# Kernel tuning notes

Measured on AMD Instinct MI355X. Metric: run time of the kernel, lower is better.

## Reference

```python
import jax, jax.numpy as jnp
import numpy as np

S, B, D, H = 2048, 2, 1024, 16
DK = D // H  # 64

def setup_inputs() -> dict:
    key0 = jax.random.key(0)
    ks = jax.random.split(key0, 11)
    scale = 0.02
    inp = {
        'query': jax.random.normal(ks[0], (S, B, D), jnp.float32),
        'key':   jax.random.normal(ks[1], (S, B, D), jnp.float32),
        'value': jax.random.normal(ks[2], (S, B, D), jnp.float32),
        # nn.Linear weights stored torch-style [out_features, in_features]
        'Wq': jax.random.normal(ks[3], (H * DK, D), jnp.float32) * scale,
        'bq': jnp.zeros((H * DK,), jnp.float32),
        'Wk': jax.random.normal(ks[4], (H * DK, D), jnp.float32) * scale,
        'bk': jnp.zeros((H * DK,), jnp.float32),
        'Wv': jax.random.normal(ks[5], (H * DK, D), jnp.float32) * scale,
        'bv': jnp.zeros((H * DK,), jnp.float32),
        'Wo': jax.random.normal(ks[6], (D, D), jnp.float32) * scale,
        'bo': jnp.zeros((D,), jnp.float32),
    }
    return inp

def _proj(x, W, b):
    # x: [S,B,D] -> [S,B,H,DK]
    y = jnp.einsum('sbd,ed->sbe', x, W) + b
    return y.reshape(x.shape[0], x.shape[1], H, DK)

def reference(query, key, value, Wq, bq, Wk, bk, Wv, bv, Wo, bo):
    q = _proj(query, Wq, bq)   # [S,B,H,DK]
    k = _proj(key,   Wk, bk)
    v = _proj(value, Wv, bv)
    # NOTE: original forward never applies self.scale -> unscaled QK^T (faithful)
    scores = jnp.einsum('ibhd,jbhd->ijbh', q, k)      # [Sq,Sk,B,H]
    attn = jax.nn.softmax(scores, axis=1)             # softmax over key axis j
    x = jnp.einsum('ijbh,jbhd->ibhd', attn, v)        # [S,B,H,DK]
    x = x.reshape(q.shape[0], q.shape[1], H * DK)     # [S,B,D]
    out = jnp.einsum('sbd,ed->sbe', x, Wo) + bo       # [S,B,D]
    return out
```

## Files before the change

### kernel.cpp

```cpp
#include <hip/hip_runtime.h>
#include <stdint.h>

#define S_LEN  2048
#define BATCH  2
#define DMODEL 1024
#define NHEAD  16
#define DKH    64

typedef __attribute__((ext_vector_type(8))) __bf16 bf16x8;
typedef __attribute__((ext_vector_type(4))) float  f32x4;
typedef unsigned short u16;
typedef unsigned int   u32;

#if __has_builtin(__builtin_amdgcn_exp2f)
#define EXP2(x) __builtin_amdgcn_exp2f(x)
#else
#define EXP2(x) __expf(0.69314718055994531f * (x))
#endif

#define SWAP32(a, b) asm("v_permlane32_swap_b32 %0, %1" : "+v"(a), "+v"(b))
#define SWAP16(a, b) asm("v_permlane16_swap_b32 %0, %1" : "+v"(a), "+v"(b))

__device__ __forceinline__ u16 f2bf(float f) {
  union { float f; u32 u; } v; v.f = f;
  u32 r = v.u + 0x7fffu + ((v.u >> 16) & 1u);
  return (u16)(r >> 16);
}

__global__ void cvt_all(const float4* __restrict__ q, const float4* __restrict__ k,
                        const float4* __restrict__ v,
                        const float4* __restrict__ wq, const float4* __restrict__ wk,
                        const float4* __restrict__ wv, const float4* __restrict__ wo,
                        ushort4* __restrict__ dst) {
  const int NX4 = (S_LEN * BATCH * DMODEL) / 4;
  const int NW4 = (DMODEL * DMODEL) / 4;
  int i = blockIdx.x * blockDim.x + threadIdx.x;
  const float4* src;
  int off;
  if (i < 3 * NX4) {
    src = (i < NX4) ? q : (i < 2 * NX4) ? k : v;
    off = i & (NX4 - 1);
  } else {
    int j = i - 3 * NX4;
    int t = j >> 18;
    src = (t == 0) ? wq : (t == 1) ? wk : (t == 2) ? wv : wo;
    off = j & (NW4 - 1);
  }
  float4 val = src[off];
  ushort4 o;
  o.x = f2bf(val.x); o.y = f2bf(val.y); o.z = f2bf(val.z); o.w = f2bf(val.w);
  dst[i] = o;
}

__global__ __launch_bounds__(256, 2)
void gemm_qkv(const u16* __restrict__ Abase, const u16* __restrict__ Wbase,
              const float* __restrict__ b0, const float* __restrict__ b1,
              const float* __restrict__ b2, u16* __restrict__ Obase) {
  __shared__ __align__(16) u16 As[128 * 32];
  __shared__ __align__(16) u16 Bs[128 * 32];

  const int L = blockIdx.x + (blockIdx.y << 3) + (blockIdx.z << 8);
  const int xcd = L & 7, sl = L >> 3;
  const int z  = sl >> 5;
  const int y  = xcd * 4 + ((sl >> 3) & 3);
  const int nx = sl & 7;

  const u16* A = Abase + (size_t)z * (S_LEN * BATCH * DMODEL);
  const u16* W = Wbase + (size_t)z * (DMODEL * DMODEL);
  const float* bias = (z == 0) ? b0 : (z == 1) ? b1 : b2;
  u16* O = Obase + (size_t)z * (S_LEN * BATCH * DMODEL);
  const float scl = (z == 0) ? 1.4426950408889634f : 1.0f;

  const int tid  = threadIdx.x;
  const int wave = tid >> 6, lane = tid & 63;
  const int quad = lane >> 4, lcol = lane & 15;
  const int m0 = y * 128, n0 = nx * 128;
  const int wm = (wave >> 1) * 64, wn = (wave & 1) * 64;

  f32x4 acc[4][4] = {};

  for (int k0 = 0; k0 < DMODEL; k0 += 32) {
#pragma unroll
    for (int r = 0; r < 2; ++r) {
      int idx = r * 256 + tid;
      int row = idx >> 2, col = (idx & 3) * 8;
      const u16* gA = A + (size_t)(m0 + row) * DMODEL + k0 + col;
      const u16* gW = W + (size_t)(n0 + row) * DMODEL + k0 + col;
      u16* lA = As + (size_t)(r * 256 + (tid & 192)) * 8;
      u16* lB = Bs + (size_t)(r * 256 + (tid & 192)) * 8;
      __builtin_amdgcn_global_load_lds((const __attribute__((address_space(1))) void*)gA,
                                       (__attribute__((address_space(3))) void*)lA, 16, 0, 0);
      __builtin_amdgcn_global_load_lds((const __attribute__((address_space(1))) void*)gW,
                                       (__attribute__((address_space(3))) void*)lB, 16, 0, 0);
    }
    __syncthreads();

    const u16* aBase = As + (wm + lcol) * 32 + quad * 8;
    const u16* bBase = Bs + (wn + lcol) * 32 + quad * 8;
    bf16x8 af[4], bfr[4];
#pragma unroll
    for (int i = 0; i < 4; ++i) af[i]  = *(const bf16x8*)(aBase + i * 16 * 32);
#pragma unroll
    for (int j = 0; j < 4; ++j) bfr[j] = *(const bf16x8*)(bBase + j * 16 * 32);
#pragma unroll
    for (int i = 0; i < 4; ++i)
#pragma unroll
      for (int j = 0; j < 4; ++j)
        acc[i][j] = __builtin_amdgcn_mfma_f32_16x16x32_bf16(af[i], bfr[j], acc[i][j], 0, 0, 0);
    __syncthreads();
  }

#pragma unroll
  for (int i = 0; i < 4; ++i) {
#pragma unroll
    for (int j = 0; j < 4; ++j) {
      int n = n0 + wn + j * 16 + lcol;
      int h = n >> 6, dk = n & 63;
      float bv = bias[n];
#pragma unroll
      for (int r = 0; r < 4; ++r) {
        int m = m0 + wm + i * 16 + quad * 4 + r;
        int s = m >> 1, b = m & 1;
        O[((size_t)(b * NHEAD + h) * S_LEN + s) * DKH + dk] = f2bf((acc[i][j][r] + bv) * scl);
      }
    }
  }
}

__global__ __launch_bounds__(256, 2)
void gemm_o(const u16* __restrict__ A, const u16* __restrict__ W,
            const float* __restrict__ bias, float* __restrict__ O) {
  __shared__ __align__(16) u16 As[128 * 32];
  __shared__ __align__(16) u16 Bs[64 * 32];

  const int L = blockIdx.x + (blockIdx.y << 4);
  const int xcd = L & 7, sl = L >> 3;
  const int y = xcd * 4 + (sl >> 4);
  const int x = sl & 15;

  const int tid  = threadIdx.x;
  const int wave = tid >> 6, lane = tid & 63;
  const int quad = lane >> 4, lcol = lane & 15;
  const int m0 = y * 128, n0 = x * 64;
  const int wm = (wave >> 1) * 64, wn = (wave & 1) * 32;

  f32x4 acc[4][2] = {};

  for (int k0 = 0; k0 < DMODEL; k0 += 32) {
#pragma unroll
    for (int r = 0; r < 2; ++r) {
      int idx = r * 256 + tid;
      int row = idx >> 2, col = (idx & 3) * 8;
      const u16* gA = A + (size_t)(m0 + row) * DMODEL + k0 + col;
      u16* lA = As + (size_t)(r * 256 + (tid & 192)) * 8;
      __builtin_amdgcn_global_load_lds((const __attribute__((address_space(1))) void*)gA,
                                       (__attribute__((address_space(3))) void*)lA, 16, 0, 0);
    }
    {
      int row = tid >> 2, col = (tid & 3) * 8;
      const u16* gW = W + (size_t)(n0 + row) * DMODEL + k0 + col;
      u16* lB = Bs + (size_t)(tid & 192) * 8;
      __builtin_amdgcn_global_load_lds((const __attribute__((address_space(1))) void*)gW,
                                       (__attribute__((address_space(3))) void*)lB, 16, 0, 0);
    }
    __syncthreads();

    const u16* aBase = As + (wm + lcol) * 32 + quad * 8;
    const u16* bBase = Bs + (wn + lcol) * 32 + quad * 8;
    bf16x8 af[4], bfr[2];
#pragma unroll
    for (int i = 0; i < 4; ++i) af[i]  = *(const bf16x8*)(aBase + i * 16 * 32);
#pragma unroll
    for (int j = 0; j < 2; ++j) bfr[j] = *(const bf16x8*)(bBase + j * 16 * 32);
#pragma unroll
    for (int i = 0; i < 4; ++i)
#pragma unroll
      for (int j = 0; j < 2; ++j)
        acc[i][j] = __builtin_amdgcn_mfma_f32_16x16x32_bf16(af[i], bfr[j], acc[i][j], 0, 0, 0);
    __syncthreads();
  }

#pragma unroll
  for (int i = 0; i < 4; ++i) {
#pragma unroll
    for (int j = 0; j < 2; ++j) {
      int n = n0 + wn + j * 16 + lcol;
      float bv = bias[n];
#pragma unroll
      for (int r = 0; r < 4; ++r) {
        int m = m0 + wm + i * 16 + quad * 4 + r;
        O[(size_t)m * DMODEL + n] = acc[i][j][r] + bv;
      }
    }
  }
}

__global__ __launch_bounds__(512, 4)
void attn_kernel(const u16* __restrict__ Q, const u16* __restrict__ K,
                 const u16* __restrict__ V, u16* __restrict__ O) {
  __shared__ __align__(16) u16 Ks[2][128 * 64];
  __shared__ __align__(16) u16 Vts[2][2 * 4608];
  __shared__ float ls2[4][2][16];

  const int tid  = threadIdx.x;
  const int wave = tid >> 6, lane = tid & 63;
  const int quad = lane >> 4, lcol = lane & 15;
  const int qg = wave & 3;
  const int kh = wave >> 2;

  const int L = blockIdx.x + (blockIdx.y << 4);
  const int xcd = L & 7, slot = L >> 3;
  const int bh = xcd * 4 + (slot >> 4);
  const int q0 = (slot & 15) * 128;

  const size_t headOff = (size_t)bh * S_LEN * DKH;
  const u16* Qg = Q + headOff;
  const u16* Kg = K + headOff;
  const u16* Vg = V + headOff;

  bf16x8 qf[2][2];
#pragma unroll
  for (int s = 0; s < 2; ++s)
#pragma unroll
    for (int kc = 0; kc < 2; ++kc)
      qf[s][kc] = *(const bf16x8*)(Qg + (size_t)(q0 + qg * 32 + s * 16 + lcol) * DKH +
                                   kc * 32 + quad * 8);

  const int krow = tid >> 3;
  const int kcs  = (((tid & 7) ^ ((tid >> 3) & 7))) * 8;
  const int kdst = (tid & 448) * 8;
  const int vhalf = lane >> 5, vkp = lane & 31, vo = wave;

  {
    const u16* vp = Vg + (size_t)(vhalf * (S_LEN / 2) + 2 * vkp) * DKH + 8 * vo;
    uint4 vr0 = *(const uint4*)vp;
    uint4 vr1 = *(const uint4*)(vp + DKH);
    __builtin_amdgcn_global_load_lds(
        (const __attribute__((address_space(1))) void*)(Kg + (size_t)krow * DKH + kcs),
        (__attribute__((address_space(3))) void*)(Ks[0] + kdst), 16, 0, 0);
    __builtin_amdgcn_global_load_lds(
        (const __attribute__((address_space(1))) void*)(Kg + (size_t)(S_LEN / 2 + krow) * DKH + kcs),
        (__attribute__((address_space(3))) void*)(Ks[0] + 4096 + kdst), 16, 0, 0);
    u16* vd = Vts[0] + vhalf * 4608;
#pragma unroll
    for (int jj = 0; jj < 4; ++jj) {
      u32 aw = ((const u32*)&vr0)[jj], bw = ((const u32*)&vr1)[jj];
      *(u32*)(vd + (size_t)(8 * vo + 2 * jj) * 72 + 2 * vkp)     = __builtin_amdgcn_perm(bw, aw, 0x05040100u);
      *(u32*)(vd + (size_t)(8 * vo + 2 * jj + 1) * 72 + 2 * vkp) = __builtin_amdgcn_perm(bw, aw, 0x07060302u);
    }
  }

  f32x4 o_acc[2][4] = {};
  float lsum[2] = {0.f, 0.f};

  for (int it = 0; it < 16; ++it) {
    const int cur = it & 1;
    __syncthreads();

    uint4 vr0, vr1;
    const bool has = (it < 15);
    if (has) {
      const int nb = (it + 1) * 64;
      const u16* vp = Vg + (size_t)(vhalf * (S_LEN / 2) + nb + 2 * vkp) * DKH + 8 * vo;
      vr0 = *(const uint4*)vp;
      vr1 = *(const uint4*)(vp + DKH);
      __builtin_amdgcn_global_load_lds(
          (const __attribute__((address_space(1))) void*)(Kg + (size_t)(nb + krow) * DKH + kcs),
          (__attribute__((address_space(3))) void*)(Ks[cur ^ 1] + kdst), 16, 0, 0);
      __builtin_amdgcn_global_load_lds(
          (const __attribute__((address_space(1))) void*)(Kg + (size_t)(S_LEN / 2 + nb + krow) * DKH + kcs),
          (__attribute__((address_space(3))) void*)(Ks[cur ^ 1] + 4096 + kdst), 16, 0, 0);
    }

    const u16* kb = Ks[cur] + kh * 4096;
    const u16* vb = Vts[cur] + kh * 4608;

#pragma unroll
    for (int g = 0; g < 2; ++g) {
      bf16x8 ak[2][2];
#pragma unroll
      for (int jb = 0; jb < 2; ++jb)
#pragma unroll
        for (int kc = 0; kc < 2; ++kc)
          ak[jb][kc] = *(const bf16x8*)(kb + (g * 32 + jb * 16 + lcol) * 64 +
                                        ((((kc << 2) | quad) ^ (lcol & 7)) << 3));
      f32x4 sc[2][2] = {};
      __builtin_amdgcn_s_setprio(1);
#pragma unroll
      for (int kc = 0; kc < 2; ++kc)
#pragma unroll
        for (int jb = 0; jb < 2; ++jb)
#pragma unroll
          for (int s = 0; s < 2; ++s)
            sc[jb][s] = __builtin_amdgcn_mfma_f32_16x16x32_bf16(ak[jb][kc], qf[s][kc], sc[jb][s], 0, 0, 0);
      __builtin_amdgcn_s_setprio(0);

      bf16x8 pa[2];
#pragma unroll
      for (int s = 0; s < 2; ++s) {
        u32 ww[2][2];
#pragma unroll
        for (int jb = 0; jb < 2; ++jb) {
          float p0 = EXP2(sc[jb][s][0]);
          float p1 = EXP2(sc[jb][s][1]);
          float p2 = EXP2(sc[jb][s][2]);
          float p3 = EXP2(sc[jb][s][3]);
          lsum[s] += (p0 + p1) + (p2 + p3);
          asm("v_cvt_pk_bf16_f32 %0, %1, %2" : "=v"(ww[jb][0]) : "v"(p0), "v"(p1));
          asm("v_cvt_pk_bf16_f32 %0, %1, %2" : "=v"(ww[jb][1]) : "v"(p2), "v"(p3));
        }
        u32 a0 = ww[0][0], b0 = ww[1][0];
        SWAP32(a0, b0); SWAP16(a0, b0);
        u32 a1 = ww[0][1], b1 = ww[1][1];
        SWAP32(a1, b1); SWAP16(a1, b1);
        union { u32 u[4]; bf16x8 v; } f;
        f.u[0] = a0; f.u[1] = a1; f.u[2] = b0; f.u[3] = b1;
        pa[s] = f.v;
      }

      bf16x8 bv[4];
#pragma unroll
      for (int jd = 0; jd < 4; ++jd)
        bv[jd] = *(const bf16x8*)(vb + (jd * 16 + lcol) * 72 + g * 32 + quad * 8);
      __builtin_amdgcn_s_setprio(1);
#pragma unroll
      for (int s = 0; s < 2; ++s)
#pragma unroll
        for (int jd = 0; jd < 4; ++jd)
          o_acc[s][jd] = __builtin_amdgcn_mfma_f32_16x16x32_bf16(pa[s], bv[jd], o_acc[s][jd], 0, 0, 0);
      __builtin_amdgcn_s_setprio(0);
    }

    if (has) {
      u16* vd = Vts[cur ^ 1] + vhalf * 4608;
#pragma unroll
      for (int jj = 0; jj < 4; ++jj) {
        u32 aw = ((const u32*)&vr0)[jj], bw = ((const u32*)&vr1)[jj];
        *(u32*)(vd + (size_t)(8 * vo + 2 * jj) * 72 + 2 * vkp)     = __builtin_amdgcn_perm(bw, aw, 0x05040100u);
        *(u32*)(vd + (size_t)(8 * vo + 2 * jj + 1) * 72 + 2 * vkp) = __builtin_amdgcn_perm(bw, aw, 0x07060302u);
      }
    }
  }

  __syncthreads();

#pragma unroll
  for (int s = 0; s < 2; ++s) {
    lsum[s] += __shfl_xor(lsum[s], 16);
    lsum[s] += __shfl_xor(lsum[s], 32);
  }

  float* scr = (float*)Vts;
  const int cbase = (qg * 64 + lane) * 36;
  if (kh == 1) {
#pragma unroll
    for (int s = 0; s < 2; ++s)
#pragma unroll
      for (int jd = 0; jd < 4; ++jd)
        *(f32x4*)(scr + cbase + (s * 4 + jd) * 4) = o_acc[s][jd];
    if (lane < 16) {
#pragma unroll
      for (int s = 0; s < 2; ++s) ls2[qg][s][lane] = lsum[s];
    }
  }
  __syncthreads();
  if (kh == 0) {
#pragma unroll
    for (int s = 0; s < 2; ++s)
#pragma unroll
      for (int jd = 0; jd < 4; ++jd)
        o_acc[s][jd] += *(const f32x4*)(scr + cbase + (s * 4 + jd) * 4);

    float tot[2];
#pragma unroll
    for (int s = 0; s < 2; ++s) tot[s] = lsum[s] + ls2[qg][s][lcol];

    const int b = bh >> 4, hh = bh & 15;
#pragma unroll
    for (int s = 0; s < 2; ++s) {
#pragma unroll
      for (int r = 0; r < 4; ++r) {
        float inv = 1.f / __shfl(tot[s], quad * 4 + r);
        int sq = q0 + qg * 32 + s * 16 + quad * 4 + r;
#pragma unroll
        for (int jd = 0; jd < 4; ++jd) {
          int dk = jd * 16 + lcol;
          O[((size_t)(sq * BATCH + b)) * DMODEL + hh * DKH + dk] = f2bf(o_acc[s][jd][r] * inv);
        }
      }
    }
  }
}

extern "C" void kernel_launch(void* const* d_in, const int* in_sizes, int n_in,
                              void* d_out, int out_size, void* d_ws, size_t ws_size,
                              hipStream_t stream) {
  const float* q  = (const float*)d_in[0];
  const float* k  = (const float*)d_in[1];
  const float* v  = (const float*)d_in[2];
  const float* Wq = (const float*)d_in[3];
  const float* bq = (const float*)d_in[4];
  const float* Wk = (const float*)d_in[5];
  const float* bk = (const float*)d_in[6];
  const float* Wv = (const float*)d_in[7];
  const float* bv = (const float*)d_in[8];
  const float* Wo = (const float*)d_in[9];
  const float* bo = (const float*)d_in[10];

  const int NX = S_LEN * BATCH * DMODEL;
  const int NW = DMODEL * DMODEL;

  u16* ws  = (u16*)d_ws;
  u16* Xq  = ws;
  u16* Wqb = Xq  + 3 * (size_t)NX;
  u16* Qb  = Wqb + 4 * (size_t)NW;
  u16* Xo  = Qb  + 3 * (size_t)NX;

  u16* Wob = Wqb + 3 * (size_t)NW;
  u16* Kb  = Qb + NX, *Vb = Qb + 2 * (size_t)NX;

  const int n4 = (3 * NX + 4 * NW) / 4;
  cvt_all<<<n4 / 256, 256, 0, stream>>>((const float4*)q, (const float4*)k, (const float4*)v,
                                        (const float4*)Wq, (const float4*)Wk, (const float4*)Wv,
                                        (const float4*)Wo, (ushort4*)ws);

  dim3 gqkv(DMODEL / 128, (S_LEN * BATCH) / 128, 3);
  gemm_qkv<<<gqkv, 256, 0, stream>>>(Xq, Wqb, bq, bk, bv, Qb);

  dim3 ga(S_LEN / 128, BATCH * NHEAD);
  attn_kernel<<<ga, 512, 0, stream>>>(Qb, Kb, Vb, Xo);

  dim3 go(DMODEL / 64, (S_LEN * BATCH) / 128);
  gemm_o<<<go, 256, 0, stream>>>(Xo, Wob, bo, (float*)d_out);
}
```

Measured before the change: 216.2 us.

## Double GEMM K-tile to 64 with XOR-swizzled LDS layout, unroll attention loop

Both projection GEMMs now stage 64-wide K tiles per iteration instead of 32. The LDS tiles use an XOR swizzle on the 16-byte chunk index so that MFMA fragment reads avoid bank conflicts. This halves the number of barrier pairs per GEMM and doubles the LDS footprint per block, which could limit occupancy. The attention main loop also gets an unroll-by-2 pragma.

```diff
diff --git a/kernel.cpp b/kernel.cpp
--- a/kernel.cpp
+++ b/kernel.cpp
@@ -56,8 +56,8 @@
 void gemm_qkv(const u16* __restrict__ Abase, const u16* __restrict__ Wbase,
               const float* __restrict__ b0, const float* __restrict__ b1,
               const float* __restrict__ b2, u16* __restrict__ Obase) {
-  __shared__ __align__(16) u16 As[128 * 32];
-  __shared__ __align__(16) u16 Bs[128 * 32];
+  __shared__ __align__(16) u16 As[128 * 64];
+  __shared__ __align__(16) u16 Bs[128 * 64];
 
   const int L = blockIdx.x + (blockIdx.y << 3) + (blockIdx.z << 8);
   const int xcd = L & 7, sl = L >> 3;
@@ -76,16 +76,19 @@
   const int quad = lane >> 4, lcol = lane & 15;
   const int m0 = y * 128, n0 = nx * 128;
   const int wm = (wave >> 1) * 64, wn = (wave & 1) * 64;
+  const int x7 = lcol & 7;
+
+  const int srow = tid >> 3;
+  const int scol = ((tid & 7) ^ ((tid >> 3) & 7)) * 8;
 
   f32x4 acc[4][4] = {};
 
-  for (int k0 = 0; k0 < DMODEL; k0 += 32) {
-#pragma unroll
-    for (int r = 0; r < 2; ++r) {
-      int idx = r * 256 + tid;
-      int row = idx >> 2, col = (idx & 3) * 8;
-      const u16* gA = A + (size_t)(m0 + row) * DMODEL + k0 + col;
-      const u16* gW = W + (size_t)(n0 + row) * DMODEL + k0 + col;
+  for (int k0 = 0; k0 < DMODEL; k0 += 64) {
+#pragma unroll
+    for (int r = 0; r < 4; ++r) {
+      int row = r * 32 + srow;
+      const u16* gA = A + (size_t)(m0 + row) * DMODEL + k0 + scol;
+      const u16* gW = W + (size_t)(n0 + row) * DMODEL + k0 + scol;
       u16* lA = As + (size_t)(r * 256 + (tid & 192)) * 8;
       u16* lB = Bs + (size_t)(r * 256 + (tid & 192)) * 8;
       __builtin_amdgcn_global_load_lds((const __attribute__((address_space(1))) void*)gA,
@@ -95,18 +98,20 @@
     }
     __syncthreads();
 
-    const u16* aBase = As + (wm + lcol) * 32 + quad * 8;
-    const u16* bBase = Bs + (wn + lcol) * 32 + quad * 8;
-    bf16x8 af[4], bfr[4];
-#pragma unroll
-    for (int i = 0; i < 4; ++i) af[i]  = *(const bf16x8*)(aBase + i * 16 * 32);
-#pragma unroll
-    for (int j = 0; j < 4; ++j) bfr[j] = *(const bf16x8*)(bBase + j * 16 * 32);
-#pragma unroll
-    for (int i = 0; i < 4; ++i)
-#pragma unroll
-      for (int j = 0; j < 4; ++j)
-        acc[i][j] = __builtin_amdgcn_mfma_f32_16x16x32_bf16(af[i], bfr[j], acc[i][j], 0, 0, 0);
+#pragma unroll
+    for (int c = 0; c < 2; ++c) {
+      const int chk = (((c << 2) | quad) ^ x7) << 3;
+      bf16x8 af[4], bfr[4];
+#pragma unroll
+      for (int i = 0; i < 4; ++i) af[i]  = *(const bf16x8*)(As + (wm + i * 16 + lcol) * 64 + chk);
+#pragma unroll
+      for (int j = 0; j < 4; ++j) bfr[j] = *(const bf16x8*)(Bs + (wn + j * 16 + lcol) * 64 + chk);
+#pragma unroll
+      for (int i = 0; i < 4; ++i)
+#pragma unroll
+        for (int j = 0; j < 4; ++j)
+          acc[i][j] = __builtin_amdgcn_mfma_f32_16x16x32_bf16(af[i], bfr[j], acc[i][j], 0, 0, 0);
+    }
     __syncthreads();
   }
 
@@ -130,8 +135,8 @@
 __global__ __launch_bounds__(256, 2)
 void gemm_o(const u16* __restrict__ A, const u16* __restrict__ W,
             const float* __restrict__ bias, float* __restrict__ O) {
-  __shared__ __align__(16) u16 As[128 * 32];
-  __shared__ __align__(16) u16 Bs[64 * 32];
+  __shared__ __align__(16) u16 As[128 * 64];
+  __shared__ __align__(16) u16 Bs[64 * 64];
 
   const int L = blockIdx.x + (blockIdx.y << 4);
   const int xcd = L & 7, sl = L >> 3;
@@ -143,40 +148,46 @@
   const int quad = lane >> 4, lcol = lane & 15;
   const int m0 = y * 128, n0 = x * 64;
   const int wm = (wave >> 1) * 64, wn = (wave & 1) * 32;
+  const int x7 = lcol & 7;
+
+  const int srow = tid >> 3;
+  const int scol = ((tid & 7) ^ ((tid >> 3) & 7)) * 8;
 
   f32x4 acc[4][2] = {};
 
-  for (int k0 = 0; k0 < DMODEL; k0 += 32) {
-#pragma unroll
-    for (int r = 0; r < 2; ++r) {
-      int idx = r * 256 + tid;
-      int row = idx >> 2, col = (idx & 3) * 8;
-      const u16* gA = A + (size_t)(m0 + row) * DMODEL + k0 + col;
+  for (int k0 = 0; k0 < DMODEL; k0 += 64) {
+#pragma unroll
+    for (int r = 0; r < 4; ++r) {
+      int row = r * 32 + srow;
+      const u16* gA = A + (size_t)(m0 + row) * DMODEL + k0 + scol;
       u16* lA = As + (size_t)(r * 256 + (tid & 192)) * 8;
       __builtin_amdgcn_global_load_lds((const __attribute__((address_space(1))) void*)gA,
                                        (__attribute__((address_space(3))) void*)lA, 16, 0, 0);
     }
-    {
-      int row = tid >> 2, col = (tid & 3) * 8;
-      const u16* gW = W + (size_t)(n0 + row) * DMODEL + k0 + col;
-      u16* lB = Bs + (size_t)(tid & 192) * 8;
+#pragma unroll
+    for (int r = 0; r < 2; ++r) {
+      int row = r * 32 + srow;
+      const u16* gW = W + (size_t)(n0 + row) * DMODEL + k0 + scol;
+      u16* lB = Bs + (size_t)(r * 256 + (tid & 192)) * 8;
       __builtin_amdgcn_global_load_lds((const __attribute__((address_space(1))) void*)gW,
                                        (__attribute__((address_space(3))) void*)lB, 16, 0, 0);
     }
     __syncthreads();
 
-    const u16* aBase = As + (wm + lcol) * 32 + quad * 8;
-    const u16* bBase = Bs + (wn + lcol) * 32 + quad * 8;
-    bf16x8 af[4], bfr[2];
-#pragma unroll
-    for (int i = 0; i < 4; ++i) af[i]  = *(const bf16x8*)(aBase + i * 16 * 32);
-#pragma unroll
-    for (int j = 0; j < 2; ++j) bfr[j] = *(const bf16x8*)(bBase + j * 16 * 32);
-#pragma unroll
-    for (int i = 0; i < 4; ++i)
-#pragma unroll
-      for (int j = 0; j < 2; ++j)
-        acc[i][j] = __builtin_amdgcn_mfma_f32_16x16x32_bf16(af[i], bfr[j], acc[i][j], 0, 0, 0);
+#pragma unroll
+    for (int c = 0; c < 2; ++c) {
+      const int chk = (((c << 2) | quad) ^ x7) << 3;
+      bf16x8 af[4], bfr[2];
+#pragma unroll
+      for (int i = 0; i < 4; ++i) af[i]  = *(const bf16x8*)(As + (wm + i * 16 + lcol) * 64 + chk);
+#pragma unroll
+      for (int j = 0; j < 2; ++j) bfr[j] = *(const bf16x8*)(Bs + (wn + j * 16 + lcol) * 64 + chk);
+#pragma unroll
+      for (int i = 0; i < 4; ++i)
+#pragma unroll
+        for (int j = 0; j < 2; ++j)
+          acc[i][j] = __builtin_amdgcn_mfma_f32_16x16x32_bf16(af[i], bfr[j], acc[i][j], 0, 0, 0);
+    }
     __syncthreads();
   }
 
@@ -253,6 +264,7 @@
   f32x4 o_acc[2][4] = {};
   float lsum[2] = {0.f, 0.f};
 
+#pragma unroll 2
   for (int it = 0; it < 16; ++it) {
     const int cur = it & 1;
     __syncthreads();
```

Result: slower. 269.1 us (+24.5%).
